# Optimization experiments

Measured on AMD Instinct MI355X. Metric: run time of the kernel, lower is better.

The kernel has to match this reference:

```python
import jax, jax.numpy as jnp
import numpy as np

D = 2048
H = 16
HD = D // H


def setup_inputs() -> dict:
    key = jax.random.key(0)
    k1, k2, k3 = jax.random.split(key, 3)
    x = jax.random.normal(k1, (2, 2048, D), dtype=jnp.float32)
    # torch Linear(d, 3d, bias=False): y = x @ W.T; store transposed weight [D, 3D]
    Wqkv = jax.random.normal(k2, (D, 3 * D), dtype=jnp.float32) * (D ** -0.5)
    Wo = jax.random.normal(k3, (D, D), dtype=jnp.float32) * (D ** -0.5)
    return {"x": x, "Wqkv": Wqkv, "Wo": Wo}


def reference(x, Wqkv, Wo):
    B, S, _ = x.shape
    qkv = (x @ Wqkv).reshape(B, S, 3, H, HD)
    q = qkv[:, :, 0].transpose(0, 2, 1, 3)  # [B,H,S,HD]
    k = qkv[:, :, 1].transpose(0, 2, 1, 3)
    v = qkv[:, :, 2].transpose(0, 2, 1, 3)
    scores = jnp.einsum("bhqd,bhkd->bhqk", q, k) * (HD ** -0.5)
    causal = jnp.tril(jnp.ones((S, S), dtype=bool))  # keep lower triangle
    scores = jnp.where(causal, scores, jnp.float32(-1e9))
    a = jax.nn.softmax(scores, axis=-1)
    o = jnp.einsum("bhqk,bhkd->bhqd", a, v)
    o = o.transpose(0, 2, 1, 3).reshape(B, S, H * HD)
    return o @ Wo
```

## Files before the change

kernel.cpp:

```cpp
#include <hip/hip_runtime.h>
#include <hip/hip_bf16.h>
#include <cstdint>

typedef __bf16 bf16;
typedef __bf16 bf16x8 __attribute__((ext_vector_type(8)));
typedef __bf16 bf16x4 __attribute__((ext_vector_type(4)));
typedef float floatx4 __attribute__((ext_vector_type(4)));

#define MFMA16(a, b, c) __builtin_amdgcn_mfma_f32_16x16x32_bf16(a, b, c, 0, 0, 0)

__device__ __forceinline__ void gload_lds16(const void* g, void* l) {
    __builtin_amdgcn_global_load_lds(
        (const __attribute__((address_space(1))) void*)g,
        (__attribute__((address_space(3))) void*)l, 16, 0, 0);
}

__global__ void downcast_kernel(const float* __restrict__ in, bf16* __restrict__ out,
                                size_t n) {
    const size_t i = ((size_t)blockIdx.x * blockDim.x + threadIdx.x) * 4;
    if (i >= n) return;
    const float4 v = *(const float4*)(in + i);
    bf16x4 o = {(bf16)v.x, (bf16)v.y, (bf16)v.z, (bf16)v.w};
    *(bf16x4*)(out + i) = o;
}

__global__ void transpose_kernel(const float* __restrict__ in, bf16* __restrict__ out,
                                 int R, int C) {
    __shared__ float tile[32][33];
    const int c0 = blockIdx.x * 32, r0 = blockIdx.y * 32;
    const int tx = threadIdx.x & 31, ty = threadIdx.x >> 5;
    for (int i = 0; i < 32; i += 8)
        tile[ty + i][tx] = in[(size_t)(r0 + ty + i) * C + (c0 + tx)];
    __syncthreads();
    for (int i = 0; i < 32; i += 8)
        out[(size_t)(c0 + ty + i) * R + (r0 + tx)] = (bf16)tile[tx][ty + i];
}

template <int MODE>
__global__ __launch_bounds__(256) void gemm_bt_kernel(
    const bf16* __restrict__ A, const bf16* __restrict__ BT,
    int M, int N, int K,
    bf16* __restrict__ qt, bf16* __restrict__ kt, bf16* __restrict__ vt,
    float* __restrict__ Cout) {
    __shared__ alignas(16) bf16 As[128 * 64];
    __shared__ alignas(16) bf16 Bs[128 * 64];

    const int tid = threadIdx.x;
    const int wave = tid >> 6, lane = tid & 63;
    const int quad = lane >> 4, r16 = lane & 15;
    const int m0 = blockIdx.y * 128, n0 = blockIdx.x * 128;
    const int wm = (wave >> 1) * 64, wn = (wave & 1) * 64;

    int srow[4], soff[4];
#pragma unroll
    for (int j = 0; j < 4; ++j) {
        const int c = tid + j * 256;
        srow[j] = c >> 3;
        soff[j] = ((c & 7) ^ (srow[j] & 7)) * 8;
    }

    floatx4 acc[4][4] = {};

    for (int k0 = 0; k0 < K; k0 += 64) {
        __syncthreads();
#pragma unroll
        for (int j = 0; j < 4; ++j) {
            const int c = tid + j * 256;
            gload_lds16(A + (size_t)(m0 + srow[j]) * K + k0 + soff[j], As + c * 8);
            gload_lds16(BT + (size_t)(n0 + srow[j]) * K + k0 + soff[j], Bs + c * 8);
        }
        __syncthreads();

#pragma unroll
        for (int kc = 0; kc < 2; ++kc) {
            bf16x8 a[4], b[4];
#pragma unroll
            for (int i = 0; i < 4; ++i) {
                const int row = wm + i * 16 + r16;
                const int sp = (4 * kc + quad) ^ (row & 7);
                a[i] = *(const bf16x8*)(As + row * 64 + sp * 8);
            }
#pragma unroll
            for (int j = 0; j < 4; ++j) {
                const int row = wn + j * 16 + r16;
                const int sp = (4 * kc + quad) ^ (row & 7);
                b[j] = *(const bf16x8*)(Bs + row * 64 + sp * 8);
            }
#pragma unroll
            for (int i = 0; i < 4; ++i)
#pragma unroll
                for (int j = 0; j < 4; ++j)
                    acc[i][j] = MFMA16(a[i], b[j], acc[i][j]);
        }
    }

    if (MODE == 0) {
        const int t = n0 >> 11;
        const float qscale = 0.08838834764831845f;
#pragma unroll
        for (int i = 0; i < 4; ++i) {
            const int mbase = m0 + wm + i * 16 + quad * 4;
            const int b_ = mbase >> 11;
            const int s = mbase & 2047;
#pragma unroll
            for (int j = 0; j < 4; ++j) {
                const int n = n0 + wn + j * 16 + r16;
                const int h = (n >> 7) & 15, hd = n & 127;
                const int bh = b_ * 16 + h;
                if (t == 0) {
#pragma unroll
                    for (int r = 0; r < 4; ++r)
                        qt[(size_t)(bh * 2048 + s + r) * 128 + hd] =
                            (bf16)(acc[i][j][r] * qscale);
                } else if (t == 1) {
#pragma unroll
                    for (int r = 0; r < 4; ++r)
                        kt[(size_t)(bh * 2048 + s + r) * 128 + hd] = (bf16)acc[i][j][r];
                } else {
                    bf16x4 pv = {(bf16)acc[i][j][0], (bf16)acc[i][j][1],
                                 (bf16)acc[i][j][2], (bf16)acc[i][j][3]};
                    *(bf16x4*)(vt + (size_t)(bh * 128 + hd) * 2048 + s) = pv;
                }
            }
        }
    } else {
#pragma unroll
        for (int i = 0; i < 4; ++i) {
            const int mbase = m0 + wm + i * 16 + quad * 4;
#pragma unroll
            for (int j = 0; j < 4; ++j) {
                const int n = n0 + wn + j * 16 + r16;
#pragma unroll
                for (int r = 0; r < 4; ++r)
                    Cout[(size_t)(mbase + r) * N + n] = acc[i][j][r];
            }
        }
    }
}

__global__ __launch_bounds__(256) void attn_kernel(
    const bf16* __restrict__ qt, const bf16* __restrict__ kt,
    const bf16* __restrict__ vt, bf16* __restrict__ o) {
    __shared__ alignas(16) bf16 Ks[2][64 * 128];
    __shared__ alignas(16) bf16 Vts[2][128 * 64];
    __shared__ alignas(16) bf16 Ps[4][16 * 72];

    const int tid = threadIdx.x;
    const int wave = tid >> 6, lane = tid & 63;
    const int quad = lane >> 4, r16 = lane & 15;
    const int pair = blockIdx.x, bh = blockIdx.y;
    const int b_ = bh >> 4, h = bh & 15;

    auto stageKV = [&](int buf, int k0) {
#pragma unroll
        for (int j = 0; j < 4; ++j) {
            const int c = tid + j * 256;
            const int row = c >> 4, sp = c & 15, s = sp ^ (row & 15);
            gload_lds16(kt + (((size_t)bh * 2048 + k0 + row) << 7) + s * 8,
                        &Ks[buf][c * 8]);
        }
#pragma unroll
        for (int j = 0; j < 4; ++j) {
            const int c = tid + j * 256;
            const int row = c >> 3, sp = c & 7, s = sp ^ (row & 7);
            gload_lds16(vt + ((size_t)bh * 128 + row) * 2048 + k0 + s * 8,
                        &Vts[buf][c * 8]);
        }
    };

    for (int half = 0; half < 2; ++half) {
        const int t = half == 0 ? pair : 31 - pair;
        const int q0 = t * 64;

        bf16x8 aq[4];
        {
            const bf16* qbase = qt + (((size_t)bh * 2048 + q0 + wave * 16 + r16) << 7);
#pragma unroll
            for (int kc = 0; kc < 4; ++kc)
                aq[kc] = *(const bf16x8*)(qbase + kc * 32 + quad * 8);
        }

        floatx4 oacc[8] = {};
        float lsum[4] = {0.f, 0.f, 0.f, 0.f};

        stageKV(0, 0);
        __syncthreads();
        int cur = 0;

        for (int it = 0; it <= t; ++it) {
            if (it < t) stageKV(cur ^ 1, (it + 1) * 64);

            const bf16* Kc = &Ks[cur][0];
            const bf16* Vc = &Vts[cur][0];

            floatx4 sacc[4] = {};
            __builtin_amdgcn_s_setprio(1);
#pragma unroll
            for (int nt = 0; nt < 4; ++nt) {
                const int row = nt * 16 + r16;
#pragma unroll
                for (int kc = 0; kc < 4; ++kc) {
                    const int sp = (4 * kc + quad) ^ r16;
                    bf16x8 bk = *(const bf16x8*)(Kc + row * 128 + sp * 8);
                    sacc[nt] = MFMA16(aq[kc], bk, sacc[nt]);
                }
            }
            __builtin_amdgcn_s_setprio(0);

            const int qrowC = q0 + wave * 16 + quad * 4;
            const int k0 = it * 64;
            float p[4][4];
            if (it == t) {
#pragma unroll
                for (int nt = 0; nt < 4; ++nt)
#pragma unroll
                    for (int r = 0; r < 4; ++r) {
                        const bool ok = (k0 + nt * 16 + r16) <= (qrowC + r);
                        const float e = ok ? __expf(sacc[nt][r]) : 0.f;
                        p[nt][r] = e;
                        lsum[r] += e;
                    }
            } else {
#pragma unroll
                for (int nt = 0; nt < 4; ++nt)
#pragma unroll
                    for (int r = 0; r < 4; ++r) {
                        const float e = __expf(sacc[nt][r]);
                        p[nt][r] = e;
                        lsum[r] += e;
                    }
            }

#pragma unroll
            for (int nt = 0; nt < 4; ++nt)
#pragma unroll
                for (int r = 0; r < 4; ++r)
                    Ps[wave][(quad * 4 + r) * 72 + nt * 16 + r16] = (bf16)p[nt][r];

            __builtin_amdgcn_s_setprio(1);
#pragma unroll
            for (int kblk = 0; kblk < 2; ++kblk) {
                bf16x8 ap = *(const bf16x8*)(&Ps[wave][r16 * 72 + kblk * 32 + quad * 8]);
#pragma unroll
                for (int nt2 = 0; nt2 < 8; ++nt2) {
                    const int row = nt2 * 16 + r16;
                    const int sp = (4 * kblk + quad) ^ (row & 7);
                    bf16x8 bv = *(const bf16x8*)(Vc + row * 64 + sp * 8);
                    oacc[nt2] = MFMA16(ap, bv, oacc[nt2]);
                }
            }
            __builtin_amdgcn_s_setprio(0);

            __syncthreads();
            cur ^= 1;
        }

#pragma unroll
        for (int r = 0; r < 4; ++r) {
            float s = lsum[r];
#pragma unroll
            for (int off = 1; off < 16; off <<= 1) s += __shfl_xor(s, off);
            lsum[r] = s;
        }

#pragma unroll
        for (int r = 0; r < 4; ++r) {
            const int qq = q0 + wave * 16 + quad * 4 + r;
            const float inv = 1.0f / lsum[r];
            bf16* orow = o + (size_t)(b_ * 2048 + qq) * 2048 + h * 128;
#pragma unroll
            for (int nt2 = 0; nt2 < 8; ++nt2)
                orow[nt2 * 16 + r16] = (bf16)(oacc[nt2][r] * inv);
        }
    }
}

extern "C" void kernel_launch(void* const* d_in, const int* in_sizes, int n_in,
                              void* d_out, int out_size, void* d_ws, size_t ws_size,
                              hipStream_t stream) {
    const float* x    = (const float*)d_in[0];
    const float* Wqkv = (const float*)d_in[1];
    const float* Wo   = (const float*)d_in[2];
    float* out        = (float*)d_out;

    char* ws = (char*)d_ws;
    bf16* xb    = (bf16*)ws; ws += (size_t)4096 * 2048 * 2;
    bf16* WqkvT = (bf16*)ws; ws += (size_t)6144 * 2048 * 2;
    bf16* WoT   = (bf16*)ws; ws += (size_t)2048 * 2048 * 2;
    bf16* qt    = (bf16*)ws; ws += (size_t)32 * 2048 * 128 * 2;
    bf16* kt    = (bf16*)ws; ws += (size_t)32 * 2048 * 128 * 2;
    bf16* vt    = (bf16*)ws; ws += (size_t)32 * 128 * 2048 * 2;
    bf16* ob    = (bf16*)ws; ws += (size_t)4096 * 2048 * 2;

    downcast_kernel<<<8192, 256, 0, stream>>>(x, xb, (size_t)4096 * 2048);
    transpose_kernel<<<dim3(192, 64), 256, 0, stream>>>(Wqkv, WqkvT, 2048, 6144);
    transpose_kernel<<<dim3(64, 64), 256, 0, stream>>>(Wo, WoT, 2048, 2048);

    gemm_bt_kernel<0><<<dim3(48, 32), 256, 0, stream>>>(
        xb, WqkvT, 4096, 6144, 2048, qt, kt, vt, nullptr);

    attn_kernel<<<dim3(16, 32), 256, 0, stream>>>(qt, kt, vt, ob);

    gemm_bt_kernel<1><<<dim3(16, 32), 256, 0, stream>>>(
        ob, WoT, 4096, 2048, 2048, nullptr, nullptr, nullptr, out);
}
```

Before: 368.0 us.

## Rework attention to 128-row query tiles with 32x32 MFMA

The attention kernel now gives each block one 128-row query tile (32 rows per wave) instead of two paired 64-row tiles, and switches from 16x16x32 to 32x32x16 bf16 MFMA for both QK^T and PV. Each K/V tile staged in LDS is reused by twice as many query rows, and the P staging buffer gets an XOR swizzle. The grid is reordered so that heavy and light causal tiles are interleaved, and launch bounds request two blocks per CU. In exchange, waves whose rows lie entirely above a diagonal KV tile sit idle during that iteration, the larger accumulators raise register pressure, and the load balancing across the causal triangle is coarser.

```diff
diff --git a/kernel.cpp b/kernel.cpp
--- a/kernel.cpp
+++ b/kernel.cpp
@@ -6,8 +6,10 @@
 typedef __bf16 bf16x8 __attribute__((ext_vector_type(8)));
 typedef __bf16 bf16x4 __attribute__((ext_vector_type(4)));
 typedef float floatx4 __attribute__((ext_vector_type(4)));
+typedef float f32x16 __attribute__((ext_vector_type(16)));
 
 #define MFMA16(a, b, c) __builtin_amdgcn_mfma_f32_16x16x32_bf16(a, b, c, 0, 0, 0)
+#define MFMA32(a, b, c) __builtin_amdgcn_mfma_f32_32x32x16_bf16(a, b, c, 0, 0, 0)
 
 __device__ __forceinline__ void gload_lds16(const void* g, void* l) {
     __builtin_amdgcn_global_load_lds(
@@ -138,18 +140,30 @@
     }
 }
 
-__global__ __launch_bounds__(256) void attn_kernel(
+__global__ __launch_bounds__(256, 2) void attn_kernel(
     const bf16* __restrict__ qt, const bf16* __restrict__ kt,
     const bf16* __restrict__ vt, bf16* __restrict__ o) {
     __shared__ alignas(16) bf16 Ks[2][64 * 128];
     __shared__ alignas(16) bf16 Vts[2][128 * 64];
-    __shared__ alignas(16) bf16 Ps[4][16 * 72];
+    __shared__ alignas(16) bf16 Ps[4][32 * 64];
 
     const int tid = threadIdx.x;
     const int wave = tid >> 6, lane = tid & 63;
-    const int quad = lane >> 4, r16 = lane & 15;
-    const int pair = blockIdx.x, bh = blockIdx.y;
-    const int b_ = bh >> 4, h = bh & 15;
+    const int l31 = lane & 31, h = lane >> 5;
+    const int bh = blockIdx.x, by = blockIdx.y;
+    const int t = by < 8 ? by : 23 - by;
+    const int b_ = bh >> 4, hh = bh & 15;
+
+    const int q0 = t * 128;
+    const int qbase = q0 + wave * 32;
+
+    bf16x8 aq[8];
+    {
+        const bf16* qrow = qt + (((size_t)bh * 2048 + qbase + l31) << 7);
+#pragma unroll
+        for (int s = 0; s < 8; ++s)
+            aq[s] = *(const bf16x8*)(qrow + s * 16 + h * 8);
+    }
 
     auto stageKV = [&](int buf, int k0) {
 #pragma unroll
@@ -168,109 +182,88 @@
         }
     };
 
-    for (int half = 0; half < 2; ++half) {
-        const int t = half == 0 ? pair : 31 - pair;
-        const int q0 = t * 64;
-
-        bf16x8 aq[4];
-        {
-            const bf16* qbase = qt + (((size_t)bh * 2048 + q0 + wave * 16 + r16) << 7);
-#pragma unroll
-            for (int kc = 0; kc < 4; ++kc)
-                aq[kc] = *(const bf16x8*)(qbase + kc * 32 + quad * 8);
-        }
-
-        floatx4 oacc[8] = {};
-        float lsum[4] = {0.f, 0.f, 0.f, 0.f};
-
-        stageKV(0, 0);
-        __syncthreads();
-        int cur = 0;
-
-        for (int it = 0; it <= t; ++it) {
-            if (it < t) stageKV(cur ^ 1, (it + 1) * 64);
-
+    f32x16 oacc[4] = {};
+    float lsum[16] = {};
+
+    const int nit = 2 * t + 2;
+    stageKV(0, 0);
+    __syncthreads();
+    int cur = 0;
+
+    for (int it = 0; it < nit; ++it) {
+        if (it + 1 < nit) stageKV(cur ^ 1, (it + 1) * 64);
+        const int k0 = it * 64;
+
+        if (k0 <= qbase + 31) {
             const bf16* Kc = &Ks[cur][0];
             const bf16* Vc = &Vts[cur][0];
 
-            floatx4 sacc[4] = {};
+            f32x16 sacc[2] = {};
             __builtin_amdgcn_s_setprio(1);
 #pragma unroll
-            for (int nt = 0; nt < 4; ++nt) {
-                const int row = nt * 16 + r16;
-#pragma unroll
-                for (int kc = 0; kc < 4; ++kc) {
-                    const int sp = (4 * kc + quad) ^ r16;
-                    bf16x8 bk = *(const bf16x8*)(Kc + row * 128 + sp * 8);
-                    sacc[nt] = MFMA16(aq[kc], bk, sacc[nt]);
+            for (int nt = 0; nt < 2; ++nt) {
+#pragma unroll
+                for (int s = 0; s < 8; ++s) {
+                    const int sp = (2 * s + h) ^ (lane & 15);
+                    bf16x8 bk = *(const bf16x8*)(Kc + (nt * 32 + l31) * 128 + sp * 8);
+                    sacc[nt] = MFMA32(aq[s], bk, sacc[nt]);
                 }
             }
             __builtin_amdgcn_s_setprio(0);
 
-            const int qrowC = q0 + wave * 16 + quad * 4;
-            const int k0 = it * 64;
-            float p[4][4];
-            if (it == t) {
-#pragma unroll
-                for (int nt = 0; nt < 4; ++nt)
-#pragma unroll
-                    for (int r = 0; r < 4; ++r) {
-                        const bool ok = (k0 + nt * 16 + r16) <= (qrowC + r);
-                        const float e = ok ? __expf(sacc[nt][r]) : 0.f;
-                        p[nt][r] = e;
-                        lsum[r] += e;
-                    }
-            } else {
-#pragma unroll
-                for (int nt = 0; nt < 4; ++nt)
-#pragma unroll
-                    for (int r = 0; r < 4; ++r) {
-                        const float e = __expf(sacc[nt][r]);
-                        p[nt][r] = e;
-                        lsum[r] += e;
-                    }
-            }
-
-#pragma unroll
-            for (int nt = 0; nt < 4; ++nt)
-#pragma unroll
-                for (int r = 0; r < 4; ++r)
-                    Ps[wave][(quad * 4 + r) * 72 + nt * 16 + r16] = (bf16)p[nt][r];
-
+            const bool needmask = (k0 + 63) > qbase;
+#pragma unroll
+            for (int nt = 0; nt < 2; ++nt) {
+                const int key = k0 + nt * 32 + l31;
+                const int seg0 = nt * 4 + (l31 >> 3);
+#pragma unroll
+                for (int r = 0; r < 16; ++r) {
+                    const int rr = (r & 3) + 8 * (r >> 2) + 4 * h;
+                    float e = __expf(sacc[nt][r]);
+                    if (needmask && (key > qbase + rr)) e = 0.f;
+                    lsum[r] += e;
+                    Ps[wave][rr * 64 + ((seg0 ^ (rr & 7)) << 3) + (l31 & 7)] = (bf16)e;
+                }
+            }
+
+            bf16x8 ap[4];
+#pragma unroll
+            for (int ks = 0; ks < 4; ++ks) {
+                const int sp = (2 * ks + h) ^ (l31 & 7);
+                ap[ks] = *(const bf16x8*)(&Ps[wave][l31 * 64 + sp * 8]);
+            }
             __builtin_amdgcn_s_setprio(1);
 #pragma unroll
-            for (int kblk = 0; kblk < 2; ++kblk) {
-                bf16x8 ap = *(const bf16x8*)(&Ps[wave][r16 * 72 + kblk * 32 + quad * 8]);
-#pragma unroll
-                for (int nt2 = 0; nt2 < 8; ++nt2) {
-                    const int row = nt2 * 16 + r16;
-                    const int sp = (4 * kblk + quad) ^ (row & 7);
-                    bf16x8 bv = *(const bf16x8*)(Vc + row * 64 + sp * 8);
-                    oacc[nt2] = MFMA16(ap, bv, oacc[nt2]);
+            for (int d0 = 0; d0 < 4; ++d0) {
+#pragma unroll
+                for (int ks = 0; ks < 4; ++ks) {
+                    const int sp = (2 * ks + h) ^ (l31 & 7);
+                    bf16x8 bv = *(const bf16x8*)(Vc + (d0 * 32 + l31) * 64 + sp * 8);
+                    oacc[d0] = MFMA32(ap[ks], bv, oacc[d0]);
                 }
             }
             __builtin_amdgcn_s_setprio(0);
-
-            __syncthreads();
-            cur ^= 1;
-        }
-
-#pragma unroll
-        for (int r = 0; r < 4; ++r) {
-            float s = lsum[r];
-#pragma unroll
-            for (int off = 1; off < 16; off <<= 1) s += __shfl_xor(s, off);
-            lsum[r] = s;
-        }
-
-#pragma unroll
-        for (int r = 0; r < 4; ++r) {
-            const int qq = q0 + wave * 16 + quad * 4 + r;
-            const float inv = 1.0f / lsum[r];
-            bf16* orow = o + (size_t)(b_ * 2048 + qq) * 2048 + h * 128;
-#pragma unroll
-            for (int nt2 = 0; nt2 < 8; ++nt2)
-                orow[nt2 * 16 + r16] = (bf16)(oacc[nt2][r] * inv);
+        }
+
+        __syncthreads();
+        cur ^= 1;
+    }
+
+#pragma unroll
+    for (int r = 0; r < 16; ++r) {
+        float s = lsum[r];
+#pragma unroll
+        for (int off = 1; off < 32; off <<= 1) s += __shfl_xor(s, off);
+        lsum[r] = 1.0f / s;
+    }
+
+#pragma unroll
+    for (int d0 = 0; d0 < 4; ++d0) {
+#pragma unroll
+        for (int r = 0; r < 16; ++r) {
+            const int rr = (r & 3) + 8 * (r >> 2) + 4 * h;
+            o[(size_t)(b_ * 2048 + qbase + rr) * 2048 + hh * 128 + d0 * 32 + l31] =
+                (bf16)(oacc[d0][r] * lsum[r]);
         }
     }
 }
@@ -299,7 +292,7 @@
     gemm_bt_kernel<0><<<dim3(48, 32), 256, 0, stream>>>(
         xb, WqkvT, 4096, 6144, 2048, qt, kt, vt, nullptr);
 
-    attn_kernel<<<dim3(16, 32), 256, 0, stream>>>(qt, kt, vt, ob);
+    attn_kernel<<<dim3(32, 16), 256, 0, stream>>>(qt, kt, vt, ob);
 
     gemm_bt_kernel<1><<<dim3(16, 32), 256, 0, stream>>>(
         ob, WoT, 4096, 2048, 2048, nullptr, nullptr, nullptr, out);
```

Result: slower. 375.8 us (+2.1%).
